# Optimization experiments

Measured on AMD Instinct MI355X. Metric: run time of the kernel, lower is better.

## Reference

```python
import jax, jax.numpy as jnp
import numpy as np

B, C, HZ, SX = 512, 112, 8, 16
P = HZ * HZ   # num_kernel = 64 template pixels
OC = 256
EPS = 1e-5

def _conv(x, w, pad, groups=1):
    return jax.lax.conv_general_dilated(
        x, w, (1, 1), [(pad, pad), (pad, pad)],
        feature_group_count=groups,
        dimension_numbers=('NCHW', 'OIHW', 'NCHW'))

def _bn(x, g, b, m, v):
    # eval-mode BatchNorm2d with running stats
    scale = (g / jnp.sqrt(v + EPS))[None, :, None, None]
    return (x - m[None, :, None, None]) * scale + b[None, :, None, None]

def setup_inputs() -> dict:
    key = jax.random.key(0)
    ks = jax.random.split(key, 16)
    n = lambda i, shape, s=0.05: jax.random.normal(ks[i], shape, dtype=jnp.float32) * s
    return dict(
        search=jax.random.normal(ks[0], (B, C, SX, SX), dtype=jnp.float32),
        kernel=jax.random.normal(ks[1], (B, C, HZ, HZ), dtype=jnp.float32),
        ca_w1=n(2, (P, P)), ca_b1=jnp.zeros((P,), jnp.float32),
        ca_w2=n(3, (P, P)), ca_b2=jnp.zeros((P,), jnp.float32),
        cls_dw=n(4, (P, 1, 3, 3)), cls_pw=n(5, (OC, P)),
        cls_bn_g=jnp.ones((OC,), jnp.float32), cls_bn_b=jnp.zeros((OC,), jnp.float32),
        cls_bn_m=n(6, (OC,)), cls_bn_v=jax.random.uniform(ks[7], (OC,), jnp.float32, 0.5, 1.5),
        cls_pred_w=n(8, (1, OC, 3, 3)), cls_pred_b=jnp.zeros((1,), jnp.float32),
        box_dw=n(9, (P, 1, 3, 3)), box_pw=n(10, (OC, P)),
        box_bn_g=jnp.ones((OC,), jnp.float32), box_bn_b=jnp.zeros((OC,), jnp.float32),
        box_bn_m=n(11, (OC,)), box_bn_v=jax.random.uniform(ks[12], (OC,), jnp.float32, 0.5, 1.5),
        box_pred_w=n(13, (4, OC, 3, 3)), box_pred_b=jnp.zeros((4,), jnp.float32),
        adjust=0.1 * jnp.ones((1,), jnp.float32),
        bias_p=jnp.ones((1, 4, 1, 1), jnp.float32),
    )

def reference(search, kernel, ca_w1, ca_b1, ca_w2, ca_b2,
              cls_dw, cls_pw, cls_bn_g, cls_bn_b, cls_bn_m, cls_bn_v,
              cls_pred_w, cls_pred_b,
              box_dw, box_pw, box_bn_g, box_bn_b, box_bn_m, box_bn_v,
              box_pred_w, box_pred_b, adjust, bias_p):
    b, c, h, w = search.shape
    # pixel-wise correlation (batched form of the per-sample F.conv2d loop):
    # corr[b,p,i,j] = sum_c kernel[b,c].flatten()[p] * search[b,c,i,j]
    z = kernel.reshape(b, c, -1)                       # [B, C, P]
    corr = jnp.einsum('bcp,bcij->bpij', z, search)      # [B, P, H, W]
    # channel attention (CAModule, reduction=1)
    s = corr.mean(axis=(2, 3))                          # [B, P]
    a = jax.nn.sigmoid(jax.nn.relu(s @ ca_w1.T + ca_b1) @ ca_w2.T + ca_b2)
    corr = corr * a[:, :, None, None]
    # cls tower: depthwise 3x3 -> pointwise -> BN -> ReLU
    cfeat = jnp.einsum('oc,bchw->bohw', cls_pw, _conv(corr, cls_dw, 1, groups=P))
    cfeat = jax.nn.relu(_bn(cfeat, cls_bn_g, cls_bn_b, cls_bn_m, cls_bn_v))
    cls = 0.1 * (_conv(cfeat, cls_pred_w, 1) + cls_pred_b[None, :, None, None])
    # bbox tower
    rfeat = jnp.einsum('oc,bchw->bohw', box_pw, _conv(corr, box_dw, 1, groups=P))
    rfeat = jax.nn.relu(_bn(rfeat, box_bn_g, box_bn_b, box_bn_m, box_bn_v))
    pred = _conv(rfeat, box_pred_w, 1) + box_pred_b[None, :, None, None]
    x = jnp.exp(adjust[0] * pred + bias_p)
    return (x, cls)
```

## Files before the change

### kernel.cpp

```cpp
#include <hip/hip_runtime.h>
#include <hip/hip_bf16.h>


typedef __attribute__((ext_vector_type(8))) short  bf16x8;
typedef __attribute__((ext_vector_type(4))) float  f32x4;

union U8 { bf16x8 v; uint4 q; unsigned short u[8]; };

__device__ __forceinline__ float bf2f(unsigned short h){
  union { unsigned int u; float f; } c; c.u = ((unsigned int)h) << 16; return c.f;
}
__device__ __forceinline__ unsigned short f2bf(float f){
  return __bfloat16_as_ushort(__float2bfloat16(f));
}
__device__ __forceinline__ unsigned int f2bf2(float lo, float hi){
  return (unsigned int)f2bf(lo) | ((unsigned int)f2bf(hi) << 16);
}

__device__ __forceinline__ int swz(int row, int pix){
  return row*256 + (((pix>>3) ^ (row&31))<<3) + (pix&7);
}
__device__ __forceinline__ int zt_off(int p, int c){
  return (p<<8) + ((((c>>3) ^ (p&15)) & 15)<<4) + ((c&7)<<1);
}
__device__ __forceinline__ int sT_off(int pix, int c){
  return (pix<<7) + ((((c>>3) ^ (pix&7) ^ ((pix>>3)&7)) & 7)<<4) + ((c&7)<<1);
}
__device__ __forceinline__ int dT_off(int pix, int p){
  return (pix<<7) + (((((p>>3) ^ pix) & 7)) << 4) + ((p & 7) << 1);
}
__device__ __forceinline__ int fT_off(int pix, int ocl){
  return (pix<<6) + ((((ocl>>3) ^ pix ^ (pix>>2)) & 3) << 4) + ((ocl & 7) << 1);
}
__device__ __forceinline__ int pA_off(int ocl, int p){
  return (ocl<<7) + (((((p>>3) ^ ocl) & 7)) << 4) + ((p & 7) << 1);
}

__device__ __forceinline__ void stage_pw(int tid, int oc0,
                                         const float* __restrict__ pw,
                                         unsigned char* __restrict__ dst){
  const int ocl = tid >> 4, p0 = (tid & 15) << 2;
  const float4 f0 = *(const float4*)&pw[(oc0 + ocl)*64 + p0];
  uint2 w; w.x = f2bf2(f0.x, f0.y); w.y = f2bf2(f0.z, f0.w);
  *(uint2*)(dst + pA_off(ocl, p0)) = w;
}

template<int NOUT>
__device__ __forceinline__ void stage_wA(int tid, int oc0,
                                         const float* __restrict__ pdw,
                                         unsigned char* __restrict__ dst){
  #pragma unroll
  for (int i=0;i<(NOUT*288+511)/512;++i){
    const int idx = i*512 + tid;
    if (idx < NOUT*288){
      const int o   = idx / 288;
      const int rem = idx - o*288;
      const int tau = rem >> 5, ocl = rem & 31;
      *(unsigned short*)(dst + (idx<<1)) =
          f2bf(pdw[(o*256 + oc0 + ocl)*9 + tau]);
    }
  }
}

template<int NOUT>
__device__ __forceinline__ void run_tower(
    int tid, float ap,
    const float* __restrict__ dw,  const float* __restrict__ pw,
    const float* __restrict__ bng, const float* __restrict__ bnb,
    const float* __restrict__ bnm, const float* __restrict__ bnv,
    const float* __restrict__ pdw, const float* __restrict__ pdb,
    float* __restrict__ outp, float adj, const float* __restrict__ biasp,
    unsigned char* smem)
{
  const int lane = tid & 63, wave = tid >> 6;
  const int l15 = lane & 15, lg = lane >> 4;
  unsigned short* sA16 = (unsigned short*)smem;

  {
    const int p = lane;
    unsigned char* dT = smem + 32768;
    float wd[9];
    #pragma unroll
    for (int k=0;k<9;++k) wd[k] = dw[p*9+k] * ap;
    #pragma unroll
    for (int io=0;io<2;++io){
      const int ir = wave*2 + io;
      float ot[16];
      #pragma unroll
      for (int j=0;j<16;++j) ot[j] = 0.f;
      #pragma unroll
      for (int dr=0;dr<3;++dr){
        const int r = ir-1+dr;
        if (r >= 0 && r < 16){
          unsigned short tr[16];
          *(uint4*)&tr[0] = *(uint4*)&sA16[swz(p, r*16)];
          *(uint4*)&tr[8] = *(uint4*)&sA16[swz(p, r*16 + 8)];
          float rr[16];
          #pragma unroll
          for (int j=0;j<16;++j) rr[j] = bf2f(tr[j]);
          const float w0 = wd[dr*3+0], w1 = wd[dr*3+1], w2 = wd[dr*3+2];
          #pragma unroll
          for (int j=0;j<16;++j){
            float s = w1*rr[j];
            if (j > 0)  s = fmaf(w0, rr[j-1], s);
            if (j < 15) s = fmaf(w2, rr[j+1], s);
            ot[j] += s;
          }
        }
      }
      #pragma unroll
      for (int j=0;j<16;++j)
        *(unsigned short*)(dT + dT_off(ir*16+j, p)) = f2bf(ot[j]);
    }
  }
  __syncthreads();

  U8 bfr[2][2];
  #pragma unroll
  for (int nt=0;nt<2;++nt)
    #pragma unroll
    for (int ks=0;ks<2;++ks)
      bfr[nt][ks].q = *(const uint4*)(smem + 32768 +
          dT_off(wave*32 + nt*16 + l15, ks*32 + lg*8));
  __syncthreads();

  float* scl = (float*)(smem + 61952);
  float* bia = (float*)(smem + 62976);
  if (tid < 256){
    const float s = bng[tid] * rsqrtf(bnv[tid] + 1e-5f);
    scl[tid] = s;
    bia[tid] = bnb[tid] - bnm[tid]*s;
  }
  stage_pw(tid, 0, pw, smem + 49152);
  stage_wA<NOUT>(tid, 0, pdw, smem + 57344);

  f32x4 accp[2];
  #pragma unroll
  for (int nt=0;nt<2;++nt) accp[nt] = f32x4{0.f,0.f,0.f,0.f};

  for (int ch=0; ch<8; ++ch){
    const int buf = ch & 1, oc0 = ch*32;
    __syncthreads();

    unsigned char* pAb = smem + 49152 + buf*4096;
    U8 af[2][2];
    #pragma unroll
    for (int mt=0;mt<2;++mt)
      #pragma unroll
      for (int ks=0;ks<2;++ks)
        af[mt][ks].q = *(const uint4*)(pAb + pA_off(mt*16 + l15, ks*32 + lg*8));
    f32x4 accw[2][2];
    #pragma unroll
    for (int mt=0;mt<2;++mt)
      #pragma unroll
      for (int nt=0;nt<2;++nt) accw[mt][nt] = f32x4{0.f,0.f,0.f,0.f};
    #pragma unroll
    for (int nt=0;nt<2;++nt){
      #pragma unroll
      for (int mt=0;mt<2;++mt){
        accw[mt][nt] = __builtin_amdgcn_mfma_f32_16x16x32_bf16(
            af[mt][0].v, bfr[nt][0].v, accw[mt][nt], 0, 0, 0);
        accw[mt][nt] = __builtin_amdgcn_mfma_f32_16x16x32_bf16(
            af[mt][1].v, bfr[nt][1].v, accw[mt][nt], 0, 0, 0);
      }
    }
    #pragma unroll
    for (int mt=0;mt<2;++mt){
      #pragma unroll
      for (int r=0;r<4;++r){
        const int ocl = mt*16 + lg*4 + r;
        const float sc = scl[oc0+ocl], bi = bia[oc0+ocl];
        #pragma unroll
        for (int nt=0;nt<2;++nt){
          const int pix = wave*32 + nt*16 + l15;
          const float v = fmaxf(fmaf(accw[mt][nt][r], sc, bi), 0.f);
          *(unsigned short*)(smem + 32768 + fT_off(pix, ocl)) = f2bf(v);
        }
      }
    }
    __syncthreads();

    unsigned char* wAb = smem + 57344 + buf*2304;
    #pragma unroll
    for (int dr=0;dr<3;++dr){
      #pragma unroll
      for (int dc=0;dc<3;++dc){
        const int tau = dr*3 + dc;
        U8 a;
        const int mr = (NOUT == 4) ? (l15 & 3) : 0;
        a.q = *(const uint4*)(wAb + ((mr*288 + tau*32 + lg*8) << 1));
        if (l15 >= NOUT) a.q = make_uint4(0u,0u,0u,0u);
        #pragma unroll
        for (int nt=0;nt<2;++nt){
          const int rp = wave*2 + nt + dr - 1;
          if (rp >= 0 && rp <= 15){
            const int cp = l15 + dc - 1;
            const int cc = cp < 0 ? 0 : (cp > 15 ? 15 : cp);
            U8 bf;
            bf.q = *(const uint4*)(smem + 32768 + fT_off(rp*16 + cc, lg*8));
            if (cp != cc) bf.q = make_uint4(0u,0u,0u,0u);
            accp[nt] = __builtin_amdgcn_mfma_f32_16x16x32_bf16(
                a.v, bf.v, accp[nt], 0, 0, 0);
          }
        }
      }
    }
    if (ch < 7){
      stage_pw(tid, oc0 + 32, pw, smem + 49152 + (buf^1)*4096);
      stage_wA<NOUT>(tid, oc0 + 32, pdw, smem + 57344 + (buf^1)*2304);
    }
  }

  if (lane < 16){
    #pragma unroll
    for (int nt=0;nt<2;++nt){
      const int rt = wave*2 + nt;
      if constexpr (NOUT == 1){
        outp[rt*16 + lane] = 0.1f*(accp[nt][0] + pdb[0]);
      } else {
        #pragma unroll
        for (int o=0;o<4;++o)
          outp[o*256 + rt*16 + lane] =
              expf(fmaf(adj, accp[nt][o] + pdb[o], biasp[o]));
      }
    }
  }
  __syncthreads();
}

__global__ __launch_bounds__(512, 4) void fused_head(
  const float* __restrict__ search, const float* __restrict__ kern,
  const float* __restrict__ ca_w1, const float* __restrict__ ca_b1,
  const float* __restrict__ ca_w2, const float* __restrict__ ca_b2,
  const float* __restrict__ cls_dw, const float* __restrict__ cls_pw,
  const float* __restrict__ cls_bn_g, const float* __restrict__ cls_bn_b,
  const float* __restrict__ cls_bn_m, const float* __restrict__ cls_bn_v,
  const float* __restrict__ cls_pred_w, const float* __restrict__ cls_pred_b,
  const float* __restrict__ box_dw, const float* __restrict__ box_pw,
  const float* __restrict__ box_bn_g, const float* __restrict__ box_bn_b,
  const float* __restrict__ box_bn_m, const float* __restrict__ box_bn_v,
  const float* __restrict__ box_pred_w, const float* __restrict__ box_pred_b,
  const float* __restrict__ adjust, const float* __restrict__ bias_p,
  float* __restrict__ out)
{
  __shared__ __align__(16) unsigned char smem[65536];
  const int b   = blockIdx.x;
  const int tid = threadIdx.x;
  const int lane = tid & 63, wave = tid >> 6;
  const int l15 = lane & 15, lg = lane >> 4;

  unsigned char* zb = smem;
  {
    const float* kb = kern + (size_t)b*7168;
    #pragma unroll
    for (int i=0;i<14;++i){
      const int idx = i*512 + tid;
      const int c = idx>>6, p = idx&63;
      *(unsigned short*)(zb + zt_off(p,c)) = f2bf(kb[idx]);
    }
    #pragma unroll
    for (int i=0;i<2;++i){
      const int idx = i*512 + tid;
      const int p = idx>>4, c = 112 + (idx&15);
      *(unsigned short*)(zb + zt_off(p,c)) = 0;
    }
  }

  unsigned char* stb = smem + 16384;
  const float* sea = search + (size_t)b*28672;
  f32x4 acc[4][2];
  #pragma unroll
  for (int mt=0;mt<4;++mt)
    #pragma unroll
    for (int nt=0;nt<2;++nt) acc[mt][nt] = f32x4{0.f,0.f,0.f,0.f};

  for (int kc=0;kc<2;++kc){
    __syncthreads();
    #pragma unroll
    for (int i=0;i<8;++i){
      const int f4i = i*512 + tid;
      const int cc = f4i>>6, pix0 = (f4i&63)<<2;
      const int c  = kc*64 + cc;
      float4 v;
      if (c < 112) v = *(const float4*)(sea + c*256 + pix0);
      else         v = make_float4(0.f,0.f,0.f,0.f);
      const float vv[4] = {v.x, v.y, v.z, v.w};
      #pragma unroll
      for (int j=0;j<4;++j)
        *(unsigned short*)(stb + sT_off(pix0+j, cc)) = f2bf(vv[j]);
    }
    __syncthreads();
    #pragma unroll
    for (int kt=0;kt<2;++kt){
      U8 bh[2];
      #pragma unroll
      for (int nt=0;nt<2;++nt){
        const int pix = wave*32 + nt*16 + l15;
        bh[nt].q = *(const uint4*)(stb + sT_off(pix, kt*32 + lg*8));
      }
      #pragma unroll
      for (int mt=0;mt<4;++mt){
        U8 ah;
        ah.q = *(const uint4*)(zb + zt_off(mt*16 + l15, kc*64 + kt*32 + lg*8));
        #pragma unroll
        for (int nt=0;nt<2;++nt)
          acc[mt][nt] = __builtin_amdgcn_mfma_f32_16x16x32_bf16(
              ah.v, bh[nt].v, acc[mt][nt], 0, 0, 0);
      }
    }
  }
  __syncthreads();

  unsigned short* sA16 = (unsigned short*)smem;
  #pragma unroll
  for (int mt=0;mt<4;++mt){
    #pragma unroll
    for (int nt=0;nt<2;++nt){
      const int pix = wave*32 + nt*16 + l15;
      #pragma unroll
      for (int r=0;r<4;++r)
        sA16[swz(mt*16 + lg*4 + r, pix)] = f2bf(acc[mt][nt][r]);
    }
  }

  float* ws    = (float*)(smem + 49152);
  float* smean = (float*)(smem + 51200);
  float* h1    = (float*)(smem + 51456);
  float* attvG = (float*)(smem + 51712);
  #pragma unroll
  for (int mt=0;mt<4;++mt){
    #pragma unroll
    for (int r=0;r<4;++r){
      float s = acc[mt][0][r] + acc[mt][1][r];
      s += __shfl_xor(s, 1, 64);
      s += __shfl_xor(s, 2, 64);
      s += __shfl_xor(s, 4, 64);
      s += __shfl_xor(s, 8, 64);
      if (l15 == 0) ws[wave*64 + mt*16 + lg*4 + r] = s;
    }
  }
  __syncthreads();
  if (tid < 64){
    float m = 0.f;
    #pragma unroll
    for (int w=0;w<8;++w) m += ws[w*64 + tid];
    smean[tid] = m * (1.f/256.f);
  }
  __syncthreads();
  if (tid < 64){
    float s = ca_b1[tid];
    const float* wr = ca_w1 + tid*64;
    #pragma unroll 8
    for (int k=0;k<64;++k) s += smean[k]*wr[k];
    h1[tid] = fmaxf(s, 0.f);
  }
  __syncthreads();
  if (tid < 64){
    float s = ca_b2[tid];
    const float* wr = ca_w2 + tid*64;
    #pragma unroll 8
    for (int k=0;k<64;++k) s += h1[k]*wr[k];
    attvG[tid] = 1.f/(1.f + expf(-s));
  }
  __syncthreads();
  const float ap = attvG[lane];
  __syncthreads();

  const float adj = adjust[0];

  run_tower<1>(tid, ap, cls_dw, cls_pw, cls_bn_g, cls_bn_b, cls_bn_m,
               cls_bn_v, cls_pred_w, cls_pred_b,
               out + 524288 + (size_t)b*256, adj, bias_p, smem);
  run_tower<4>(tid, ap, box_dw, box_pw, box_bn_g, box_bn_b, box_bn_m,
               box_bn_v, box_pred_w, box_pred_b,
               out + (size_t)b*1024, adj, bias_p, smem);
}

extern "C" void kernel_launch(void* const* d_in, const int* in_sizes, int n_in,
                              void* d_out, int out_size, void* d_ws, size_t ws_size,
                              hipStream_t stream) {
  (void)in_sizes; (void)n_in; (void)d_ws; (void)ws_size; (void)out_size;
  const float* search     = (const float*)d_in[0];
  const float* kern       = (const float*)d_in[1];
  const float* ca_w1      = (const float*)d_in[2];
  const float* ca_b1      = (const float*)d_in[3];
  const float* ca_w2      = (const float*)d_in[4];
  const float* ca_b2      = (const float*)d_in[5];
  const float* cls_dw     = (const float*)d_in[6];
  const float* cls_pw     = (const float*)d_in[7];
  const float* cls_bn_g   = (const float*)d_in[8];
  const float* cls_bn_b   = (const float*)d_in[9];
  const float* cls_bn_m   = (const float*)d_in[10];
  const float* cls_bn_v   = (const float*)d_in[11];
  const float* cls_pred_w = (const float*)d_in[12];
  const float* cls_pred_b = (const float*)d_in[13];
  const float* box_dw     = (const float*)d_in[14];
  const float* box_pw     = (const float*)d_in[15];
  const float* box_bn_g   = (const float*)d_in[16];
  const float* box_bn_b   = (const float*)d_in[17];
  const float* box_bn_m   = (const float*)d_in[18];
  const float* box_bn_v   = (const float*)d_in[19];
  const float* box_pred_w = (const float*)d_in[20];
  const float* box_pred_b = (const float*)d_in[21];
  const float* adjust     = (const float*)d_in[22];
  const float* bias_p     = (const float*)d_in[23];

  hipLaunchKernelGGL(fused_head, dim3(512), dim3(512), 0, stream,
    search, kern, ca_w1, ca_b1, ca_w2, ca_b2,
    cls_dw, cls_pw, cls_bn_g, cls_bn_b, cls_bn_m, cls_bn_v,
    cls_pred_w, cls_pred_b,
    box_dw, box_pw, box_bn_g, box_bn_b, box_bn_m, box_bn_v,
    box_pred_w, box_pred_b, adjust, bias_p,
    (float*)d_out);
}
```

Before: 68.47 us.

## Split towers and software-pipeline box tower pointwise and pred conv stages

```diff
diff --git a/kernel.cpp b/kernel.cpp
--- a/kernel.cpp
+++ b/kernel.cpp
@@ -62,15 +62,13 @@
   }
 }
 
-template<int NOUT>
-__device__ __forceinline__ void run_tower(
+__device__ __forceinline__ void run_tower_cls(
     int tid, float ap,
     const float* __restrict__ dw,  const float* __restrict__ pw,
     const float* __restrict__ bng, const float* __restrict__ bnb,
     const float* __restrict__ bnm, const float* __restrict__ bnv,
     const float* __restrict__ pdw, const float* __restrict__ pdb,
-    float* __restrict__ outp, float adj, const float* __restrict__ biasp,
-    unsigned char* smem)
+    float* __restrict__ outp, unsigned char* smem)
 {
   const int lane = tid & 63, wave = tid >> 6;
   const int l15 = lane & 15, lg = lane >> 4;
@@ -113,8 +111,6 @@
         *(unsigned short*)(dT + dT_off(ir*16+j, p)) = f2bf(ot[j]);
     }
   }
-  __syncthreads();
-
   U8 bfr[2][2];
   #pragma unroll
   for (int nt=0;nt<2;++nt)
@@ -132,64 +128,47 @@
     bia[tid] = bnb[tid] - bnm[tid]*s;
   }
   stage_pw(tid, 0, pw, smem + 49152);
-  stage_wA<NOUT>(tid, 0, pdw, smem + 57344);
+  stage_wA<1>(tid, 0, pdw, smem + 57344);
 
   f32x4 accp[2];
-  #pragma unroll
-  for (int nt=0;nt<2;++nt) accp[nt] = f32x4{0.f,0.f,0.f,0.f};
+  accp[0] = f32x4{0.f,0.f,0.f,0.f};
+  accp[1] = f32x4{0.f,0.f,0.f,0.f};
 
   for (int ch=0; ch<8; ++ch){
     const int buf = ch & 1, oc0 = ch*32;
     __syncthreads();
-
     unsigned char* pAb = smem + 49152 + buf*4096;
-    U8 af[2][2];
-    #pragma unroll
-    for (int mt=0;mt<2;++mt)
-      #pragma unroll
-      for (int ks=0;ks<2;++ks)
-        af[mt][ks].q = *(const uint4*)(pAb + pA_off(mt*16 + l15, ks*32 + lg*8));
-    f32x4 accw[2][2];
-    #pragma unroll
-    for (int mt=0;mt<2;++mt)
-      #pragma unroll
-      for (int nt=0;nt<2;++nt) accw[mt][nt] = f32x4{0.f,0.f,0.f,0.f};
-    #pragma unroll
-    for (int nt=0;nt<2;++nt){
-      #pragma unroll
-      for (int mt=0;mt<2;++mt){
-        accw[mt][nt] = __builtin_amdgcn_mfma_f32_16x16x32_bf16(
-            af[mt][0].v, bfr[nt][0].v, accw[mt][nt], 0, 0, 0);
-        accw[mt][nt] = __builtin_amdgcn_mfma_f32_16x16x32_bf16(
-            af[mt][1].v, bfr[nt][1].v, accw[mt][nt], 0, 0, 0);
-      }
-    }
     #pragma unroll
     for (int mt=0;mt<2;++mt){
+      U8 af0, af1;
+      af0.q = *(const uint4*)(pAb + pA_off(mt*16 + l15, lg*8));
+      af1.q = *(const uint4*)(pAb + pA_off(mt*16 + l15, 32 + lg*8));
+      f32x4 aw0 = f32x4{0.f,0.f,0.f,0.f};
+      f32x4 aw1 = f32x4{0.f,0.f,0.f,0.f};
+      aw0 = __builtin_amdgcn_mfma_f32_16x16x32_bf16(af0.v, bfr[0][0].v, aw0, 0,0,0);
+      aw0 = __builtin_amdgcn_mfma_f32_16x16x32_bf16(af1.v, bfr[0][1].v, aw0, 0,0,0);
+      aw1 = __builtin_amdgcn_mfma_f32_16x16x32_bf16(af0.v, bfr[1][0].v, aw1, 0,0,0);
+      aw1 = __builtin_amdgcn_mfma_f32_16x16x32_bf16(af1.v, bfr[1][1].v, aw1, 0,0,0);
       #pragma unroll
       for (int r=0;r<4;++r){
         const int ocl = mt*16 + lg*4 + r;
         const float sc = scl[oc0+ocl], bi = bia[oc0+ocl];
-        #pragma unroll
-        for (int nt=0;nt<2;++nt){
-          const int pix = wave*32 + nt*16 + l15;
-          const float v = fmaxf(fmaf(accw[mt][nt][r], sc, bi), 0.f);
-          *(unsigned short*)(smem + 32768 + fT_off(pix, ocl)) = f2bf(v);
-        }
+        *(unsigned short*)(smem + 32768 + fT_off(wave*32 + l15, ocl)) =
+            f2bf(fmaxf(fmaf(aw0[r], sc, bi), 0.f));
+        *(unsigned short*)(smem + 32768 + fT_off(wave*32 + 16 + l15, ocl)) =
+            f2bf(fmaxf(fmaf(aw1[r], sc, bi), 0.f));
       }
     }
     __syncthreads();
-
-    unsigned char* wAb = smem + 57344 + buf*2304;
+    unsigned char* wAb = smem + 57344 + buf*576;
     #pragma unroll
     for (int dr=0;dr<3;++dr){
       #pragma unroll
       for (int dc=0;dc<3;++dc){
         const int tau = dr*3 + dc;
         U8 a;
-        const int mr = (NOUT == 4) ? (l15 & 3) : 0;
-        a.q = *(const uint4*)(wAb + ((mr*288 + tau*32 + lg*8) << 1));
-        if (l15 >= NOUT) a.q = make_uint4(0u,0u,0u,0u);
+        a.q = *(const uint4*)(wAb + ((tau*32 + lg*8) << 1));
+        if (l15 >= 1) a.q = make_uint4(0u,0u,0u,0u);
         #pragma unroll
         for (int nt=0;nt<2;++nt){
           const int rp = wave*2 + nt + dr - 1;
@@ -207,7 +186,7 @@
     }
     if (ch < 7){
       stage_pw(tid, oc0 + 32, pw, smem + 49152 + (buf^1)*4096);
-      stage_wA<NOUT>(tid, oc0 + 32, pdw, smem + 57344 + (buf^1)*2304);
+      stage_wA<1>(tid, oc0 + 32, pdw, smem + 57344 + (buf^1)*576);
     }
   }
 
@@ -215,17 +194,183 @@
     #pragma unroll
     for (int nt=0;nt<2;++nt){
       const int rt = wave*2 + nt;
-      if constexpr (NOUT == 1){
-        outp[rt*16 + lane] = 0.1f*(accp[nt][0] + pdb[0]);
-      } else {
+      outp[rt*16 + lane] = 0.1f*(accp[nt][0] + pdb[0]);
+    }
+  }
+  __syncthreads();
+}
+
+__device__ __forceinline__ void run_tower_box(
+    int tid, float ap,
+    const float* __restrict__ dw,  const float* __restrict__ pw,
+    const float* __restrict__ bng, const float* __restrict__ bnb,
+    const float* __restrict__ bnm, const float* __restrict__ bnv,
+    const float* __restrict__ pdw, const float* __restrict__ pdb,
+    float* __restrict__ outp, float adj, const float* __restrict__ biasp,
+    unsigned char* smem)
+{
+  const int lane = tid & 63, wave = tid >> 6;
+  const int l15 = lane & 15, lg = lane >> 4;
+  unsigned short* sA16 = (unsigned short*)smem;
+
+  {
+    const int p = lane;
+    unsigned char* dT = smem + 32768;
+    float wd[9];
+    #pragma unroll
+    for (int k=0;k<9;++k) wd[k] = dw[p*9+k] * ap;
+    #pragma unroll
+    for (int io=0;io<2;++io){
+      const int ir = wave*2 + io;
+      float ot[16];
+      #pragma unroll
+      for (int j=0;j<16;++j) ot[j] = 0.f;
+      #pragma unroll
+      for (int dr=0;dr<3;++dr){
+        const int r = ir-1+dr;
+        if (r >= 0 && r < 16){
+          unsigned short tr[16];
+          *(uint4*)&tr[0] = *(uint4*)&sA16[swz(p, r*16)];
+          *(uint4*)&tr[8] = *(uint4*)&sA16[swz(p, r*16 + 8)];
+          float rr[16];
+          #pragma unroll
+          for (int j=0;j<16;++j) rr[j] = bf2f(tr[j]);
+          const float w0 = wd[dr*3+0], w1 = wd[dr*3+1], w2 = wd[dr*3+2];
+          #pragma unroll
+          for (int j=0;j<16;++j){
+            float s = w1*rr[j];
+            if (j > 0)  s = fmaf(w0, rr[j-1], s);
+            if (j < 15) s = fmaf(w2, rr[j+1], s);
+            ot[j] += s;
+          }
+        }
+      }
+      #pragma unroll
+      for (int j=0;j<16;++j)
+        *(unsigned short*)(dT + dT_off(ir*16+j, p)) = f2bf(ot[j]);
+    }
+  }
+  U8 bfr[2][2];
+  #pragma unroll
+  for (int nt=0;nt<2;++nt)
+    #pragma unroll
+    for (int ks=0;ks<2;++ks)
+      bfr[nt][ks].q = *(const uint4*)(smem + 32768 +
+          dT_off(wave*32 + nt*16 + l15, ks*32 + lg*8));
+  __syncthreads();
+
+  float* scl = (float*)(smem + 61952);
+  float* bia = (float*)(smem + 62976);
+  if (tid < 256){
+    const float s = bng[tid] * rsqrtf(bnv[tid] + 1e-5f);
+    scl[tid] = s;
+    bia[tid] = bnb[tid] - bnm[tid]*s;
+  }
+  stage_pw(tid, 0,  pw, smem + 49152);
+  stage_pw(tid, 32, pw, smem + 53248);
+  stage_wA<4>(tid, 0, pdw, smem + 57344);
+  __syncthreads();
+
+  f32x4 accp[2];
+  accp[0] = f32x4{0.f,0.f,0.f,0.f};
+  accp[1] = f32x4{0.f,0.f,0.f,0.f};
+
+  {
+    unsigned char* pAb = smem + 49152;
+    #pragma unroll
+    for (int mt=0;mt<2;++mt){
+      U8 af0, af1;
+      af0.q = *(const uint4*)(pAb + pA_off(mt*16 + l15, lg*8));
+      af1.q = *(const uint4*)(pAb + pA_off(mt*16 + l15, 32 + lg*8));
+      f32x4 aw0 = f32x4{0.f,0.f,0.f,0.f};
+      f32x4 aw1 = f32x4{0.f,0.f,0.f,0.f};
+      aw0 = __builtin_amdgcn_mfma_f32_16x16x32_bf16(af0.v, bfr[0][0].v, aw0, 0,0,0);
+      aw0 = __builtin_amdgcn_mfma_f32_16x16x32_bf16(af1.v, bfr[0][1].v, aw0, 0,0,0);
+      aw1 = __builtin_amdgcn_mfma_f32_16x16x32_bf16(af0.v, bfr[1][0].v, aw1, 0,0,0);
+      aw1 = __builtin_amdgcn_mfma_f32_16x16x32_bf16(af1.v, bfr[1][1].v, aw1, 0,0,0);
+      #pragma unroll
+      for (int r=0;r<4;++r){
+        const int ocl = mt*16 + lg*4 + r;
+        const float sc = scl[ocl], bi = bia[ocl];
+        *(unsigned short*)(smem + fT_off(wave*32 + l15, ocl)) =
+            f2bf(fmaxf(fmaf(aw0[r], sc, bi), 0.f));
+        *(unsigned short*)(smem + fT_off(wave*32 + 16 + l15, ocl)) =
+            f2bf(fmaxf(fmaf(aw1[r], sc, bi), 0.f));
+      }
+    }
+  }
+  __syncthreads();
+
+  for (int i=0; i<8; ++i){
+    const int par = i & 1;
+    if (i < 6) stage_pw(tid, (i+2)*32, pw, smem + 49152 + par*4096);
+    if (i < 7) stage_wA<4>(tid, (i+1)*32, pdw, smem + 57344 + (par^1)*2304);
+    if (i < 7){
+      unsigned char* pAb   = smem + 49152 + (par^1)*4096;
+      unsigned char* featw = smem + ((par^1)<<14);
+      const int oc0 = (i+1)*32;
+      #pragma unroll
+      for (int mt=0;mt<2;++mt){
+        U8 af0, af1;
+        af0.q = *(const uint4*)(pAb + pA_off(mt*16 + l15, lg*8));
+        af1.q = *(const uint4*)(pAb + pA_off(mt*16 + l15, 32 + lg*8));
+        f32x4 aw0 = f32x4{0.f,0.f,0.f,0.f};
+        f32x4 aw1 = f32x4{0.f,0.f,0.f,0.f};
+        aw0 = __builtin_amdgcn_mfma_f32_16x16x32_bf16(af0.v, bfr[0][0].v, aw0, 0,0,0);
+        aw0 = __builtin_amdgcn_mfma_f32_16x16x32_bf16(af1.v, bfr[0][1].v, aw0, 0,0,0);
+        aw1 = __builtin_amdgcn_mfma_f32_16x16x32_bf16(af0.v, bfr[1][0].v, aw1, 0,0,0);
+        aw1 = __builtin_amdgcn_mfma_f32_16x16x32_bf16(af1.v, bfr[1][1].v, aw1, 0,0,0);
         #pragma unroll
-        for (int o=0;o<4;++o)
-          outp[o*256 + rt*16 + lane] =
-              expf(fmaf(adj, accp[nt][o] + pdb[o], biasp[o]));
-      }
-    }
-  }
-  __syncthreads();
+        for (int r=0;r<4;++r){
+          const int ocl = mt*16 + lg*4 + r;
+          const float sc = scl[oc0+ocl], bi = bia[oc0+ocl];
+          *(unsigned short*)(featw + fT_off(wave*32 + l15, ocl)) =
+              f2bf(fmaxf(fmaf(aw0[r], sc, bi), 0.f));
+          *(unsigned short*)(featw + fT_off(wave*32 + 16 + l15, ocl)) =
+              f2bf(fmaxf(fmaf(aw1[r], sc, bi), 0.f));
+        }
+      }
+    }
+    {
+      unsigned char* featr = smem + (par<<14);
+      unsigned char* wAb   = smem + 57344 + par*2304;
+      #pragma unroll
+      for (int dr=0;dr<3;++dr){
+        #pragma unroll
+        for (int dc=0;dc<3;++dc){
+          const int tau = dr*3 + dc;
+          U8 a;
+          a.q = *(const uint4*)(wAb + (((l15&3)*288 + tau*32 + lg*8) << 1));
+          if (l15 >= 4) a.q = make_uint4(0u,0u,0u,0u);
+          #pragma unroll
+          for (int nt=0;nt<2;++nt){
+            const int rp = wave*2 + nt + dr - 1;
+            if (rp >= 0 && rp <= 15){
+              const int cp = l15 + dc - 1;
+              const int cc = cp < 0 ? 0 : (cp > 15 ? 15 : cp);
+              U8 bf;
+              bf.q = *(const uint4*)(featr + fT_off(rp*16 + cc, lg*8));
+              if (cp != cc) bf.q = make_uint4(0u,0u,0u,0u);
+              accp[nt] = __builtin_amdgcn_mfma_f32_16x16x32_bf16(
+                  a.v, bf.v, accp[nt], 0, 0, 0);
+            }
+          }
+        }
+      }
+    }
+    __syncthreads();
+  }
+
+  if (lane < 16){
+    #pragma unroll
+    for (int nt=0;nt<2;++nt){
+      const int rt = wave*2 + nt;
+      #pragma unroll
+      for (int o=0;o<4;++o)
+        outp[o*256 + rt*16 + lane] =
+            expf(fmaf(adj, accp[nt][o] + pdb[o], biasp[o]));
+    }
+  }
 }
 
 __global__ __launch_bounds__(512, 4) void fused_head(
@@ -368,12 +513,12 @@
 
   const float adj = adjust[0];
 
-  run_tower<1>(tid, ap, cls_dw, cls_pw, cls_bn_g, cls_bn_b, cls_bn_m,
-               cls_bn_v, cls_pred_w, cls_pred_b,
-               out + 524288 + (size_t)b*256, adj, bias_p, smem);
-  run_tower<4>(tid, ap, box_dw, box_pw, box_bn_g, box_bn_b, box_bn_m,
-               box_bn_v, box_pred_w, box_pred_b,
-               out + (size_t)b*1024, adj, bias_p, smem);
+  run_tower_cls(tid, ap, cls_dw, cls_pw, cls_bn_g, cls_bn_b, cls_bn_m,
+                cls_bn_v, cls_pred_w, cls_pred_b,
+                out + 524288 + (size_t)b*256, smem);
+  run_tower_box(tid, ap, box_dw, box_pw, box_bn_g, box_bn_b, box_bn_m,
+                box_bn_v, box_pred_w, box_pred_b,
+                out + (size_t)b*1024, adj, bias_p, smem);
 }
 
 extern "C" void kernel_launch(void* const* d_in, const int* in_sizes, int n_in,
```

After: 73.67 us. 7.6% more time.
